# Performance work log

Hardware: AMD Instinct MI355X
Metric: run time of the kernel (lower is better)

## Reference

```python
import jax, jax.numpy as jnp
import numpy as np

INPUT_SIZE = 256
HIDDEN_SIZE = 256


def _linear_params(key, in_dim, out_dim):
    # PyTorch nn.Linear default init: U(-1/sqrt(in_dim), 1/sqrt(in_dim))
    k1, k2 = jax.random.split(key)
    bound = 1.0 / np.sqrt(in_dim)
    W = jax.random.uniform(k1, (out_dim, in_dim), jnp.float32, -bound, bound)
    b = jax.random.uniform(k2, (out_dim,), jnp.float32, -bound, bound)
    return W, b


def setup_inputs() -> dict:
    key = jax.random.key(0)
    keys = jax.random.split(key, 7)
    B = 65536
    x = jax.random.normal(keys[0], (B, INPUT_SIZE), jnp.float32)
    h_prev = jax.random.normal(keys[1], (B, HIDDEN_SIZE), jnp.float32)
    W_ir, b_ir = _linear_params(keys[2], INPUT_SIZE, HIDDEN_SIZE)
    W_iz, b_iz = _linear_params(keys[3], INPUT_SIZE, HIDDEN_SIZE)
    W_in, b_in = _linear_params(keys[4], INPUT_SIZE, HIDDEN_SIZE)
    W_hz, b_hz = _linear_params(keys[5], HIDDEN_SIZE, HIDDEN_SIZE)
    W_hn, b_hn = _linear_params(keys[6], HIDDEN_SIZE, HIDDEN_SIZE)
    # NOTE: weights_hr exists in the torch module but is never used in forward
    # (the source uses weights_hz for the reset gate too), so it is omitted.
    return {
        'x': x, 'h_prev': h_prev,
        'W_ir': W_ir, 'b_ir': b_ir,
        'W_iz': W_iz, 'b_iz': b_iz,
        'W_in': W_in, 'b_in': b_in,
        'W_hz': W_hz, 'b_hz': b_hz,
        'W_hn': W_hn, 'b_hn': b_hn,
    }


def reference(x, h_prev, W_ir, b_ir, W_iz, b_iz, W_in, b_in, W_hz, b_hz, W_hn, b_hn):
    # Faithful to source: both z and r use the hz projection of h_prev.
    hz = h_prev @ W_hz.T + b_hz                       # [B, H]
    z = jax.nn.sigmoid(x @ W_iz.T + b_iz + hz)        # update gate
    r = jax.nn.sigmoid(x @ W_ir.T + b_ir + hz)        # reset gate (bug: uses hz)
    g = jnp.tanh(x @ W_in.T + b_in + r * (h_prev @ W_hn.T + b_hn))
    h_new = (1.0 - z) * g + z * h_prev
    return h_new
```

## Files before the change

### kernel.cpp

```cpp
#include <hip/hip_runtime.h>
#include <hip/hip_bf16.h>

typedef __bf16 bf16x8 __attribute__((ext_vector_type(8)));
typedef __bf16 bf16x4 __attribute__((ext_vector_type(4)));
typedef float  f32x4  __attribute__((ext_vector_type(4)));

#define HID   256
#define BM    64
#define PITCH 264

__global__ void __launch_bounds__(256) prepack_frag(
    const float* __restrict__ w0, const float* __restrict__ w1,
    const float* __restrict__ w2, const float* __restrict__ w3,
    const float* __restrict__ w4, __bf16* __restrict__ wb)
{
    int t    = blockIdx.x * 256 + threadIdx.x;
    int lane = t & 63;
    int cb   = (t >> 6) & 15;
    int gk   = t >> 10;
    int g    = gk % 5;
    int ks   = gk / 5;
    const float* W = g == 0 ? w0 : g == 1 ? w1 : g == 2 ? w2 : g == 3 ? w3 : w4;
    int row = cb * 16 + (lane & 15);
    int k0  = ks * 32 + (lane >> 4) * 8;
    float4 p = *(const float4*)(W + row * HID + k0);
    float4 q = *(const float4*)(W + row * HID + k0 + 4);
    bf16x8 o;
    o[0]=(__bf16)p.x; o[1]=(__bf16)p.y; o[2]=(__bf16)p.z; o[3]=(__bf16)p.w;
    o[4]=(__bf16)q.x; o[5]=(__bf16)q.y; o[6]=(__bf16)q.z; o[7]=(__bf16)q.w;
    *(bf16x8*)(wb + (size_t)t * 8) = o;
}

#define MFMA1(D, A_, B_) D = __builtin_amdgcn_mfma_f32_16x16x32_bf16(A_, B_, D, 0, 0, 0)

#define MFMA12(MF, AX, AH, B_) do {                                   \
    _Pragma("unroll")                                                 \
    for (int nf = 0; nf < 2; ++nf) {                                  \
        MFMA1(az[MF][nf],  AX, B_[2 + nf]);                           \
        MFMA1(az[MF][nf],  AH, B_[6 + nf]);                           \
        MFMA1(ar[MF][nf],  AX, B_[0 + nf]);                           \
        MFMA1(ar[MF][nf],  AH, B_[6 + nf]);                           \
        MFMA1(anx[MF][nf], AX, B_[4 + nf]);                           \
        MFMA1(anh[MF][nf], AH, B_[8 + nf]);                           \
    }                                                                 \
} while (0)

#define LOADB(DST, KK) do {                                           \
    _Pragma("unroll")                                                 \
    for (int g = 0; g < 5; ++g)                                       \
        _Pragma("unroll")                                             \
        for (int nf = 0; nf < 2; ++nf)                                \
            DST[g * 2 + nf] =                                         \
                *(const bf16x8*)(wbase + ((KK) * 5 + g) * 8192 + nf * 512); \
} while (0)

#define LOADB_SLOW(DST, KK) do {                                      \
    _Pragma("unroll")                                                 \
    for (int g = 0; g < 5; ++g)                                       \
        _Pragma("unroll")                                             \
        for (int nf = 0; nf < 2; ++nf) {                              \
            const float* pp = wsrc[g] + ((wn * 2 + nf) * 16 + lr) * HID + (KK) * 32 + lg * 8; \
            float4 c0 = *(const float4*)(pp), c1 = *(const float4*)(pp + 4); \
            bf16x8 u;                                                 \
            u[0]=(__bf16)c0.x; u[1]=(__bf16)c0.y; u[2]=(__bf16)c0.z; u[3]=(__bf16)c0.w; \
            u[4]=(__bf16)c1.x; u[5]=(__bf16)c1.y; u[6]=(__bf16)c1.z; u[7]=(__bf16)c1.w; \
            DST[g * 2 + nf] = u;                                      \
        }                                                             \
} while (0)

#define CLUSTER(B_, KC) do {                                          \
    const int kb = (KC) * 32 + lg * 8;                                \
    bf16x8 a0x = *(const bf16x8*)(xt + (0 * 16 + lr) * PITCH + kb);   \
    bf16x8 a0h = *(const bf16x8*)(ht + (0 * 16 + lr) * PITCH + kb);   \
    bf16x8 a1x = *(const bf16x8*)(xt + (1 * 16 + lr) * PITCH + kb);   \
    bf16x8 a1h = *(const bf16x8*)(ht + (1 * 16 + lr) * PITCH + kb);   \
    MFMA12(0, a0x, a0h, B_);                                          \
    a0x = *(const bf16x8*)(xt + (2 * 16 + lr) * PITCH + kb);          \
    a0h = *(const bf16x8*)(ht + (2 * 16 + lr) * PITCH + kb);          \
    MFMA12(1, a1x, a1h, B_);                                          \
    a1x = *(const bf16x8*)(xt + (3 * 16 + lr) * PITCH + kb);          \
    a1h = *(const bf16x8*)(ht + (3 * 16 + lr) * PITCH + kb);          \
    MFMA12(2, a0x, a0h, B_);                                          \
    MFMA12(3, a1x, a1h, B_);                                          \
} while (0)

template<bool PACKED>
__global__ void __launch_bounds__(512, 2) gru_fused(
    const float* __restrict__ x,  const float* __restrict__ h,
    const __bf16* __restrict__ wb,
    const float* __restrict__ w_ir, const float* __restrict__ w_iz,
    const float* __restrict__ w_in, const float* __restrict__ w_hz,
    const float* __restrict__ w_hn,
    const float* __restrict__ b_ir, const float* __restrict__ b_iz,
    const float* __restrict__ b_in, const float* __restrict__ b_hz,
    const float* __restrict__ b_hn,
    float* __restrict__ out)
{
    __shared__ __bf16 xt[BM * PITCH];
    __shared__ __bf16 ht[BM * PITCH];

    const int t    = threadIdx.x;
    const int row0 = blockIdx.x * BM;
    const int lane = t & 63;
    const int wn   = t >> 6;
    const int lr   = lane & 15;
    const int lg   = lane >> 4;

    const float* wsrc[5] = { w_ir, w_iz, w_in, w_hz, w_hn };
    const __bf16* wbase = wb + wn * 1024 + lane * 8;

    float4 vx[8], vh[8];
#pragma unroll
    for (int i = 0; i < 8; ++i) {
        int c = i * 512 + t, r = c >> 6, k4 = (c & 63) * 4;
        vx[i] = *(const float4*)(x + (size_t)(row0 + r) * HID + k4);
        vh[i] = *(const float4*)(h + (size_t)(row0 + r) * HID + k4);
    }
    bf16x8 Ba[10], Bb[10];
    if (PACKED) LOADB(Ba, wn);
#pragma unroll
    for (int i = 0; i < 8; ++i) {
        int c = i * 512 + t, r = c >> 6, k4 = (c & 63) * 4;
        bf16x4 bx, bh;
        bx[0] = (__bf16)vx[i].x; bx[1] = (__bf16)vx[i].y; bx[2] = (__bf16)vx[i].z; bx[3] = (__bf16)vx[i].w;
        bh[0] = (__bf16)vh[i].x; bh[1] = (__bf16)vh[i].y; bh[2] = (__bf16)vh[i].z; bh[3] = (__bf16)vh[i].w;
        *(bf16x4*)(xt + r * PITCH + k4) = bx;
        *(bf16x4*)(ht + r * PITCH + k4) = bh;
    }
    __syncthreads();

    f32x4 az[4][2], ar[4][2], anx[4][2], anh[4][2];
#pragma unroll
    for (int mf = 0; mf < 4; ++mf)
#pragma unroll
        for (int nf = 0; nf < 2; ++nf) {
            az[mf][nf] = (f32x4)0.0f; ar[mf][nf] = (f32x4)0.0f;
            anx[mf][nf] = (f32x4)0.0f; anh[mf][nf] = (f32x4)0.0f;
        }

#pragma unroll
    for (int i2 = 0; i2 < 4; ++i2) {
        const int kA = (wn + 2 * i2)     & 7;
        const int kB = (wn + 2 * i2 + 1) & 7;
        const int kN = (wn + 2 * i2 + 2) & 7;
        if (PACKED) LOADB(Bb, kB); else LOADB_SLOW(Ba, kA);
        CLUSTER(Ba, kA);
        if (PACKED) { if (i2 < 3) LOADB(Ba, kN); } else LOADB_SLOW(Bb, kB);
        CLUSTER(Bb, kB);
    }

    float bz[2], br[2], bnx[2], bnh[2];
#pragma unroll
    for (int nf = 0; nf < 2; ++nf) {
        int col = wn * 32 + nf * 16 + lr;
        bz[nf]  = b_iz[col] + b_hz[col];
        br[nf]  = b_ir[col] + b_hz[col];
        bnx[nf] = b_in[col];
        bnh[nf] = b_hn[col];
    }
#pragma unroll
    for (int mf = 0; mf < 4; ++mf)
#pragma unroll
        for (int nf = 0; nf < 2; ++nf)
#pragma unroll
            for (int i = 0; i < 4; ++i) {
                int rl  = mf * 16 + lg * 4 + i;
                int col = wn * 32 + nf * 16 + lr;
                float z  = 1.0f / (1.0f + __expf(-(az[mf][nf][i] + bz[nf])));
                float r  = 1.0f / (1.0f + __expf(-(ar[mf][nf][i] + br[nf])));
                float e2 = __expf(2.0f * (anx[mf][nf][i] + bnx[nf] + r * (anh[mf][nf][i] + bnh[nf])));
                float g  = 1.0f - 2.0f / (e2 + 1.0f);
                float hp = (float)ht[rl * PITCH + col];
                out[(size_t)(row0 + rl) * HID + col] = (1.0f - z) * g + z * hp;
            }
}

extern "C" void kernel_launch(void* const* d_in, const int* in_sizes, int n_in,
                              void* d_out, int out_size, void* d_ws, size_t ws_size,
                              hipStream_t stream) {
    const float* x    = (const float*)d_in[0];
    const float* h    = (const float*)d_in[1];
    const float* w_ir = (const float*)d_in[2];
    const float* b_ir = (const float*)d_in[3];
    const float* w_iz = (const float*)d_in[4];
    const float* b_iz = (const float*)d_in[5];
    const float* w_in = (const float*)d_in[6];
    const float* b_in = (const float*)d_in[7];
    const float* w_hz = (const float*)d_in[8];
    const float* b_hz = (const float*)d_in[9];
    const float* w_hn = (const float*)d_in[10];
    const float* b_hn = (const float*)d_in[11];
    float* out = (float*)d_out;

    const int B = in_sizes[0] / HID;
    const size_t wb_bytes = (size_t)5 * HID * HID * sizeof(__bf16);

    if (ws_size >= wb_bytes) {
        __bf16* wb = (__bf16*)d_ws;
        prepack_frag<<<160, 256, 0, stream>>>(w_ir, w_iz, w_in, w_hz, w_hn, wb);
        gru_fused<true><<<B / BM, 512, 0, stream>>>(
            x, h, wb, nullptr, nullptr, nullptr, nullptr, nullptr,
            b_ir, b_iz, b_in, b_hz, b_hn, out);
    } else {
        gru_fused<false><<<B / BM, 512, 0, stream>>>(
            x, h, nullptr, w_ir, w_iz, w_in, w_hz, w_hn,
            b_ir, b_iz, b_in, b_hz, b_hn, out);
    }
}
```

Baseline: 102.0 us.

## Double row tile to 128 and split waves into row and column groups

Raises the block row tile from 64 to 128 rows. The eight waves are arranged as 2 row groups by 4 column groups, and each wave processes the 256 output columns in two sequential halves, so every packed weight fragment is reused across twice as many rows. Inside each group the MFMA order is also changed so the three x-projection MFMAs are issued before the h-projection ones. The cost is twice the LDS per block (about 135 KB), which likely allows only one block per CU instead of two, and half as many blocks in the grid.

```diff
diff --git a/kernel.cpp b/kernel.cpp
--- a/kernel.cpp
+++ b/kernel.cpp
@@ -6,7 +6,7 @@
 typedef float  f32x4  __attribute__((ext_vector_type(4)));
 
 #define HID   256
-#define BM    64
+#define BM    128
 #define PITCH 264
 
 __global__ void __launch_bounds__(256) prepack_frag(
@@ -37,29 +37,30 @@
     _Pragma("unroll")                                                 \
     for (int nf = 0; nf < 2; ++nf) {                                  \
         MFMA1(az[MF][nf],  AX, B_[2 + nf]);                           \
+        MFMA1(ar[MF][nf],  AX, B_[0 + nf]);                           \
+        MFMA1(anx[MF][nf], AX, B_[4 + nf]);                           \
         MFMA1(az[MF][nf],  AH, B_[6 + nf]);                           \
-        MFMA1(ar[MF][nf],  AX, B_[0 + nf]);                           \
         MFMA1(ar[MF][nf],  AH, B_[6 + nf]);                           \
-        MFMA1(anx[MF][nf], AX, B_[4 + nf]);                           \
         MFMA1(anh[MF][nf], AH, B_[8 + nf]);                           \
     }                                                                 \
 } while (0)
 
-#define LOADB(DST, KK) do {                                           \
+#define LOADB(DST, KK, CS) do {                                       \
     _Pragma("unroll")                                                 \
     for (int g = 0; g < 5; ++g)                                       \
         _Pragma("unroll")                                             \
         for (int nf = 0; nf < 2; ++nf)                                \
-            DST[g * 2 + nf] =                                         \
-                *(const bf16x8*)(wbase + ((KK) * 5 + g) * 8192 + nf * 512); \
-} while (0)
-
-#define LOADB_SLOW(DST, KK) do {                                      \
+            DST[g * 2 + nf] = *(const bf16x8*)(wbase +                \
+                (((KK) * 5 + g) * 16 + (CS) * 8 + nf) * 512);         \
+} while (0)
+
+#define LOADB_SLOW(DST, KK, CS) do {                                  \
     _Pragma("unroll")                                                 \
     for (int g = 0; g < 5; ++g)                                       \
         _Pragma("unroll")                                             \
         for (int nf = 0; nf < 2; ++nf) {                              \
-            const float* pp = wsrc[g] + ((wn * 2 + nf) * 16 + lr) * HID + (KK) * 32 + lg * 8; \
+            int cb = (CS) * 8 + cg * 2 + nf;                          \
+            const float* pp = wsrc[g] + (cb * 16 + lr) * HID + (KK) * 32 + lg * 8; \
             float4 c0 = *(const float4*)(pp), c1 = *(const float4*)(pp + 4); \
             bf16x8 u;                                                 \
             u[0]=(__bf16)c0.x; u[1]=(__bf16)c0.y; u[2]=(__bf16)c0.z; u[3]=(__bf16)c0.w; \
@@ -70,16 +71,16 @@
 
 #define CLUSTER(B_, KC) do {                                          \
     const int kb = (KC) * 32 + lg * 8;                                \
-    bf16x8 a0x = *(const bf16x8*)(xt + (0 * 16 + lr) * PITCH + kb);   \
-    bf16x8 a0h = *(const bf16x8*)(ht + (0 * 16 + lr) * PITCH + kb);   \
-    bf16x8 a1x = *(const bf16x8*)(xt + (1 * 16 + lr) * PITCH + kb);   \
-    bf16x8 a1h = *(const bf16x8*)(ht + (1 * 16 + lr) * PITCH + kb);   \
+    bf16x8 a0x = *(const bf16x8*)(xt + (rbase + 0 * 16 + lr) * PITCH + kb); \
+    bf16x8 a0h = *(const bf16x8*)(ht + (rbase + 0 * 16 + lr) * PITCH + kb); \
+    bf16x8 a1x = *(const bf16x8*)(xt + (rbase + 1 * 16 + lr) * PITCH + kb); \
+    bf16x8 a1h = *(const bf16x8*)(ht + (rbase + 1 * 16 + lr) * PITCH + kb); \
     MFMA12(0, a0x, a0h, B_);                                          \
-    a0x = *(const bf16x8*)(xt + (2 * 16 + lr) * PITCH + kb);          \
-    a0h = *(const bf16x8*)(ht + (2 * 16 + lr) * PITCH + kb);          \
+    a0x = *(const bf16x8*)(xt + (rbase + 2 * 16 + lr) * PITCH + kb);  \
+    a0h = *(const bf16x8*)(ht + (rbase + 2 * 16 + lr) * PITCH + kb);  \
     MFMA12(1, a1x, a1h, B_);                                          \
-    a1x = *(const bf16x8*)(xt + (3 * 16 + lr) * PITCH + kb);          \
-    a1h = *(const bf16x8*)(ht + (3 * 16 + lr) * PITCH + kb);          \
+    a1x = *(const bf16x8*)(xt + (rbase + 3 * 16 + lr) * PITCH + kb);  \
+    a1h = *(const bf16x8*)(ht + (rbase + 3 * 16 + lr) * PITCH + kb);  \
     MFMA12(2, a0x, a0h, B_);                                          \
     MFMA12(3, a1x, a1h, B_);                                          \
 } while (0)
@@ -103,76 +104,90 @@
     const int row0 = blockIdx.x * BM;
     const int lane = t & 63;
     const int wn   = t >> 6;
+    const int rg   = wn >> 2;
+    const int cg   = wn & 3;
     const int lr   = lane & 15;
     const int lg   = lane >> 4;
+    const int rbase = rg * 64;
 
     const float* wsrc[5] = { w_ir, w_iz, w_in, w_hz, w_hn };
-    const __bf16* wbase = wb + wn * 1024 + lane * 8;
-
-    float4 vx[8], vh[8];
-#pragma unroll
-    for (int i = 0; i < 8; ++i) {
-        int c = i * 512 + t, r = c >> 6, k4 = (c & 63) * 4;
-        vx[i] = *(const float4*)(x + (size_t)(row0 + r) * HID + k4);
-        vh[i] = *(const float4*)(h + (size_t)(row0 + r) * HID + k4);
-    }
+    const __bf16* wbase = wb + cg * 1024 + lane * 8;
+
     bf16x8 Ba[10], Bb[10];
-    if (PACKED) LOADB(Ba, wn);
-#pragma unroll
-    for (int i = 0; i < 8; ++i) {
-        int c = i * 512 + t, r = c >> 6, k4 = (c & 63) * 4;
-        bf16x4 bx, bh;
-        bx[0] = (__bf16)vx[i].x; bx[1] = (__bf16)vx[i].y; bx[2] = (__bf16)vx[i].z; bx[3] = (__bf16)vx[i].w;
-        bh[0] = (__bf16)vh[i].x; bh[1] = (__bf16)vh[i].y; bh[2] = (__bf16)vh[i].z; bh[3] = (__bf16)vh[i].w;
-        *(bf16x4*)(xt + r * PITCH + k4) = bx;
-        *(bf16x4*)(ht + r * PITCH + k4) = bh;
+    if (PACKED) LOADB(Ba, wn, 0);
+
+#pragma unroll
+    for (int grp = 0; grp < 2; ++grp) {
+        float4 vx[8], vh[8];
+#pragma unroll
+        for (int i = 0; i < 8; ++i) {
+            int c = (grp * 8 + i) * 512 + t, r = c >> 6, k4 = (c & 63) * 4;
+            vx[i] = *(const float4*)(x + (size_t)(row0 + r) * HID + k4);
+            vh[i] = *(const float4*)(h + (size_t)(row0 + r) * HID + k4);
+        }
+#pragma unroll
+        for (int i = 0; i < 8; ++i) {
+            int c = (grp * 8 + i) * 512 + t, r = c >> 6, k4 = (c & 63) * 4;
+            bf16x4 bx, bh;
+            bx[0]=(__bf16)vx[i].x; bx[1]=(__bf16)vx[i].y; bx[2]=(__bf16)vx[i].z; bx[3]=(__bf16)vx[i].w;
+            bh[0]=(__bf16)vh[i].x; bh[1]=(__bf16)vh[i].y; bh[2]=(__bf16)vh[i].z; bh[3]=(__bf16)vh[i].w;
+            *(bf16x4*)(xt + r * PITCH + k4) = bx;
+            *(bf16x4*)(ht + r * PITCH + k4) = bh;
+        }
     }
     __syncthreads();
 
     f32x4 az[4][2], ar[4][2], anx[4][2], anh[4][2];
-#pragma unroll
-    for (int mf = 0; mf < 4; ++mf)
+
+#pragma unroll
+    for (int cs = 0; cs < 2; ++cs) {
+#pragma unroll
+        for (int mf = 0; mf < 4; ++mf)
+#pragma unroll
+            for (int nf = 0; nf < 2; ++nf) {
+                az[mf][nf] = (f32x4)0.0f; ar[mf][nf] = (f32x4)0.0f;
+                anx[mf][nf] = (f32x4)0.0f; anh[mf][nf] = (f32x4)0.0f;
+            }
+        if (cs == 1 && PACKED) LOADB(Ba, wn, 1);
+
+#pragma unroll
+        for (int i2 = 0; i2 < 4; ++i2) {
+            const int kA = (wn + 2 * i2)     & 7;
+            const int kB = (wn + 2 * i2 + 1) & 7;
+            const int kN = (wn + 2 * i2 + 2) & 7;
+            if (PACKED) LOADB(Bb, kB, cs); else LOADB_SLOW(Ba, kA, cs);
+            CLUSTER(Ba, kA);
+            if (PACKED) {
+                if (i2 < 3) LOADB(Ba, kN, cs);
+            } else LOADB_SLOW(Bb, kB, cs);
+            CLUSTER(Bb, kB);
+        }
+
+        float bz[2], br[2], bnx[2], bnh[2];
 #pragma unroll
         for (int nf = 0; nf < 2; ++nf) {
-            az[mf][nf] = (f32x4)0.0f; ar[mf][nf] = (f32x4)0.0f;
-            anx[mf][nf] = (f32x4)0.0f; anh[mf][nf] = (f32x4)0.0f;
-        }
-
-#pragma unroll
-    for (int i2 = 0; i2 < 4; ++i2) {
-        const int kA = (wn + 2 * i2)     & 7;
-        const int kB = (wn + 2 * i2 + 1) & 7;
-        const int kN = (wn + 2 * i2 + 2) & 7;
-        if (PACKED) LOADB(Bb, kB); else LOADB_SLOW(Ba, kA);
-        CLUSTER(Ba, kA);
-        if (PACKED) { if (i2 < 3) LOADB(Ba, kN); } else LOADB_SLOW(Bb, kB);
-        CLUSTER(Bb, kB);
+            int col = cs * 128 + cg * 32 + nf * 16 + lr;
+            bz[nf]  = b_iz[col] + b_hz[col];
+            br[nf]  = b_ir[col] + b_hz[col];
+            bnx[nf] = b_in[col];
+            bnh[nf] = b_hn[col];
+        }
+#pragma unroll
+        for (int mf = 0; mf < 4; ++mf)
+#pragma unroll
+            for (int nf = 0; nf < 2; ++nf)
+#pragma unroll
+                for (int i = 0; i < 4; ++i) {
+                    int rl  = rbase + mf * 16 + lg * 4 + i;
+                    int col = cs * 128 + cg * 32 + nf * 16 + lr;
+                    float z  = 1.0f / (1.0f + __expf(-(az[mf][nf][i] + bz[nf])));
+                    float r  = 1.0f / (1.0f + __expf(-(ar[mf][nf][i] + br[nf])));
+                    float e2 = __expf(2.0f * (anx[mf][nf][i] + bnx[nf] + r * (anh[mf][nf][i] + bnh[nf])));
+                    float g  = 1.0f - 2.0f / (e2 + 1.0f);
+                    float hp = (float)ht[rl * PITCH + col];
+                    out[(size_t)(row0 + rl) * HID + col] = (1.0f - z) * g + z * hp;
+                }
     }
-
-    float bz[2], br[2], bnx[2], bnh[2];
-#pragma unroll
-    for (int nf = 0; nf < 2; ++nf) {
-        int col = wn * 32 + nf * 16 + lr;
-        bz[nf]  = b_iz[col] + b_hz[col];
-        br[nf]  = b_ir[col] + b_hz[col];
-        bnx[nf] = b_in[col];
-        bnh[nf] = b_hn[col];
-    }
-#pragma unroll
-    for (int mf = 0; mf < 4; ++mf)
-#pragma unroll
-        for (int nf = 0; nf < 2; ++nf)
-#pragma unroll
-            for (int i = 0; i < 4; ++i) {
-                int rl  = mf * 16 + lg * 4 + i;
-                int col = wn * 32 + nf * 16 + lr;
-                float z  = 1.0f / (1.0f + __expf(-(az[mf][nf][i] + bz[nf])));
-                float r  = 1.0f / (1.0f + __expf(-(ar[mf][nf][i] + br[nf])));
-                float e2 = __expf(2.0f * (anx[mf][nf][i] + bnx[nf] + r * (anh[mf][nf][i] + bnh[nf])));
-                float g  = 1.0f - 2.0f / (e2 + 1.0f);
-                float hp = (float)ht[rl * PITCH + col];
-                out[(size_t)(row0 + rl) * HID + col] = (1.0f - z) * g + z * hp;
-            }
 }
 
 extern "C" void kernel_launch(void* const* d_in, const int* in_sizes, int n_in,
```

Result: slower. 107.6 us (+5.5%).
